# Kernel optimization log

Measured on AMD Instinct MI355X. Metric: run time of the kernel, lower is better.

## Reference

```python
import jax, jax.numpy as jnp
import numpy as np


def _wn(v, g):
    # weight norm over input axis: w[:, j] = g[j] * v[:, j] / ||v[:, j]||
    norm = jnp.sqrt(jnp.sum(v * v, axis=0, keepdims=True))
    return v * (g[None, :] / norm)


def setup_inputs() -> dict:
    key = jax.random.key(0)
    ks = jax.random.split(key, 6)
    M, K1, H, OUT = 65536, 512, 1024, 512
    x = jax.random.normal(ks[0], (M, K1), dtype=jnp.float32)
    v1 = jax.random.normal(ks[1], (K1, H), dtype=jnp.float32) * 0.05
    v2 = jax.random.normal(ks[2], (H, H), dtype=jnp.float32) * 0.05
    v3 = jax.random.normal(ks[3], (H, H), dtype=jnp.float32) * 0.05
    v4 = jax.random.normal(ks[4], (H, H), dtype=jnp.float32) * 0.05
    v5 = jax.random.normal(ks[5], (H, OUT), dtype=jnp.float32) * 0.05
    g1 = jnp.ones((H,), jnp.float32)
    g2 = jnp.ones((H,), jnp.float32)
    g3 = jnp.ones((H,), jnp.float32)
    g4 = jnp.ones((H,), jnp.float32)
    g5 = jnp.ones((OUT,), jnp.float32)
    return {"x": x, "v1": v1, "g1": g1, "v2": v2, "g2": g2,
            "v3": v3, "g3": g3, "v4": v4, "g4": g4, "v5": v5, "g5": g5}


def reference(x, v1, g1, v2, g2, v3, g3, v4, g4, v5, g5):
    w1 = _wn(v1, g1)
    w2 = _wn(v2, g2)
    w3 = _wn(v3, g3)
    w4 = _wn(v4, g4)
    w5 = _wn(v5, g5)
    h1 = jax.nn.softplus(x @ w1)    # [M, H]
    h2 = jax.nn.softplus(h1 @ w2)
    h3 = jax.nn.softplus(h2 @ w3)
    h4 = jax.nn.softplus(h3 @ w4)
    out = h4 @ w5                   # final layer linear
    return out
```

## Files before the change

### kernel.cpp

```cpp
#include <hip/hip_runtime.h>
#include <hip/hip_bf16.h>
#include <cstdint>

typedef unsigned short u16;
typedef __attribute__((ext_vector_type(8))) _Float16 f16x8;
typedef __attribute__((ext_vector_type(4))) float f32x4;
typedef __attribute__((ext_vector_type(8))) unsigned short u16x8;

typedef const __attribute__((address_space(1))) void* gas1p;
typedef __attribute__((address_space(3))) void* las3p;

__device__ __forceinline__ void gld_lds16(const void* g, void* l) {
    __builtin_amdgcn_global_load_lds((gas1p)g, (las3p)l, 16, 0, 0);
}

__device__ __forceinline__ u16 f2h(float f) {
    _Float16 h = (_Float16)f;
    return __builtin_bit_cast(u16, h);
}

__global__ void cvt_x_kernel(const float4* __restrict__ x, u16* __restrict__ xb) {
    size_t i = (size_t)blockIdx.x * blockDim.x + threadIdx.x;
    float4 a = x[2 * i];
    float4 b = x[2 * i + 1];
    u16x8 o;
    o[0] = f2h(a.x); o[1] = f2h(a.y); o[2] = f2h(a.z); o[3] = f2h(a.w);
    o[4] = f2h(b.x); o[5] = f2h(b.y); o[6] = f2h(b.z); o[7] = f2h(b.w);
    *(u16x8*)&xb[i * 8] = o;
}

struct WnDesc {
    const float* v; const float* g; u16* wT; float* partial;
    int K; int N; int blk0;
};
struct WnPack { WnDesc d[5]; int nlayer; };

__global__ void wn_partial_all(WnPack p) {
    int b = blockIdx.x;
    int l = 0;
    while (l + 1 < p.nlayer && b >= p.d[l + 1].blk0) l++;
    const WnDesc& d = p.d[l];
    int lb = b - d.blk0;
    int nbx = d.N >> 6;
    int bx = lb % nbx, seg = lb / nbx;

    int lane = threadIdx.x & 63;
    int tr = threadIdx.x >> 6;
    int n = bx * 64 + lane;
    int kseg = d.K >> 3;
    int kbeg = seg * kseg;
    float s = 0.f;
    for (int k = kbeg + tr; k < kbeg + kseg; k += 4) {
        float x = d.v[(size_t)k * d.N + n];
        s += x * x;
    }
    __shared__ float red[4][64];
    red[tr][lane] = s;
    __syncthreads();
    if (tr == 0)
        d.partial[seg * d.N + n] = red[0][lane] + red[1][lane] + red[2][lane] + red[3][lane];
}

__global__ void wn_write_all(WnPack p) {
    int b = blockIdx.x;
    int l = 0;
    while (l + 1 < p.nlayer && b >= p.d[l + 1].blk0) l++;
    const WnDesc& d = p.d[l];
    int lb = b - d.blk0;
    int nbx = d.N >> 6;
    int bx = lb % nbx, seg = lb / nbx;

    int lane = threadIdx.x & 63;
    int tr = threadIdx.x >> 6;
    int n = bx * 64 + lane;
    float s = 0.f;
#pragma unroll
    for (int i = 0; i < 8; i++) s += d.partial[i * d.N + n];
    float sc = d.g[n] / sqrtf(s);

    int kseg = d.K >> 3;
    int kbeg = seg * kseg;
    for (int k = kbeg + tr; k < kbeg + kseg; k += 4)
        d.wT[(size_t)n * d.K + k] = f2h(d.v[(size_t)k * d.N + n] * sc);
}

template<int N, int K, bool ACT, bool OUTF32>
__global__ __launch_bounds__(512, 2) void gemm_mlp(
    const u16* __restrict__ A, const u16* __restrict__ Bt,
    u16* __restrict__ Ch, float* __restrict__ Cf)
{
    constexpr int M = 65536;
    constexpr int NT = K / 64;
    constexpr int J = NT / 2;
    constexpr int NTN = N / 256;
    constexpr int NWG = (M / 256) * NTN;

    __shared__ u16 sA[2][256 * 64];
    __shared__ u16 sB[2][2 * 128 * 64];

    const int bid = blockIdx.x;
    const int wk = (bid & 7) * (NWG >> 3) + (bid >> 3);
    const int tm = wk / NTN, tn = wk % NTN;
    const long m0 = (long)tm * 256;
    const int n0 = tn * 256;

    const int tid = threadIdx.x;
    const int lane = tid & 63;
    const int wid = tid >> 6;
    const int wm = (wid >> 2) * 128;
    const int wn = (wid & 3) * 64;

    const int r8 = tid >> 3;
    const int gcol = ((tid & 7) ^ (r8 & 7)) * 8;
    const u16* Abase = A + (m0 + r8) * (size_t)K + gcol;
    const u16* Bbase = Bt + (size_t)(n0 + ((r8 >> 5) * 64 + (r8 & 31))) * K + gcol;
    const int dst8 = tid * 8;

    const u16* Aq0 = Abase;
    const u16* Aq1 = Abase + (size_t)64 * K;
    const u16* Aq2 = Abase + (size_t)128 * K;
    const u16* Aq3 = Abase + (size_t)192 * K;
    const u16* B00 = Bbase;
    const u16* B01 = Bbase + (size_t)128 * K;
    const u16* B10 = Bbase + (size_t)32 * K;
    const u16* B11 = Bbase + (size_t)160 * K;

    auto stA = [&](int buf, const u16* base, int t, int q) {
        gld_lds16(base + (size_t)t * 64, &sA[buf][q * 4096 + dst8]);
    };
    auto stB = [&](int buf, const u16* base, int t, int s, int c) {
        gld_lds16(base + (size_t)t * 64, &sB[buf][s * 8192 + c * 4096 + dst8]);
    };
    auto stA0 = [&](int buf, int t) { stA(buf, Aq0, t, 0); stA(buf, Aq2, t, 2); };
    auto stA1 = [&](int buf, int t) { stA(buf, Aq1, t, 1); stA(buf, Aq3, t, 3); };
    auto stB0 = [&](int buf, int t) { stB(buf, B00, t, 0, 0); stB(buf, B01, t, 0, 1); };
    auto stB1 = [&](int buf, int t) { stB(buf, B10, t, 1, 0); stB(buf, B11, t, 1, 1); };

    const int rbase = lane & 15;
    const int co0 = ((lane >> 4) ^ (lane & 7)) * 8;
    const int arow0 = (wm + rbase) * 64 + co0;
    const int brow0 = ((wn >> 6) * 32 + rbase) * 64 + co0;

    f32x4 acc[8][4] = {};
    f16x8 a[4][2], bq[2][2][2];

    auto ldA = [&](int buf, int qm) {
#pragma unroll
        for (int i = 0; i < 4; i++) {
            int base = arow0 + (qm * 64 + i * 16) * 64;
            a[i][0] = *(const f16x8*)&sA[buf][base];
            a[i][1] = *(const f16x8*)&sA[buf][base ^ 32];
        }
    };
    auto ldB = [&](int buf, int qn) {
#pragma unroll
        for (int j2 = 0; j2 < 2; j2++) {
            int base = brow0 + qn * 8192 + j2 * 1024;
            bq[qn][j2][0] = *(const f16x8*)&sB[buf][base];
            bq[qn][j2][1] = *(const f16x8*)&sB[buf][base ^ 32];
        }
    };
    auto mmaq = [&](int qm, int qn) {
        __builtin_amdgcn_s_setprio(1);
#pragma unroll
        for (int kk = 0; kk < 2; kk++)
#pragma unroll
            for (int i = 0; i < 4; i++)
#pragma unroll
                for (int j2 = 0; j2 < 2; j2++)
                    acc[qm * 4 + i][qn * 2 + j2] = __builtin_amdgcn_mfma_f32_16x16x32_f16(
                        a[i][kk], bq[qn][j2][kk], acc[qm * 4 + i][qn * 2 + j2], 0, 0, 0);
        __builtin_amdgcn_s_setprio(0);
    };
    auto bar = [&]() {
        asm volatile("" ::: "memory");
        __builtin_amdgcn_s_barrier();
        asm volatile("" ::: "memory");
    };

    stA0(0, 0); stB0(0, 0); stB1(0, 0); stA1(0, 0);
    stA0(1, 1); stB0(1, 1); stB1(1, 1); stA1(1, 1);
    asm volatile("s_waitcnt vmcnt(8)" ::: "memory");
    bar();

    for (int j = 0; j < J; j++) {
        const int ta = 2 * j, tb = ta + 1;
        const bool tail = (j > 0);
        const bool full = (j + 1 < J);

        if (tail) stB1(1, tb);
        ldA(0, 0); ldB(0, 0);
        bar();
        mmaq(0, 0);
        if (tail) stA1(1, tb);
        ldB(0, 1);
        bar();
        mmaq(0, 1);
        if (full) stA0(0, ta + 2);
        ldA(0, 1);
        bar();
        mmaq(1, 0);
        if (full) {
            stB0(0, ta + 2);
            asm volatile("s_waitcnt vmcnt(4)" ::: "memory");
        } else {
            asm volatile("s_waitcnt vmcnt(0)" ::: "memory");
        }
        bar();
        mmaq(1, 1);

        if (full) stB1(0, ta + 2);
        ldA(1, 0); ldB(1, 0);
        bar();
        mmaq(0, 0);
        if (full) stA1(0, ta + 2);
        ldB(1, 1);
        bar();
        mmaq(0, 1);
        if (full) stA0(1, tb + 2);
        ldA(1, 1);
        bar();
        mmaq(1, 0);
        if (full) {
            stB0(1, tb + 2);
            asm volatile("s_waitcnt vmcnt(4)" ::: "memory");
            bar();
        }
        mmaq(1, 1);
    }

    const long crow0 = m0 + wm + ((lane >> 4) << 2);
    const int ccol0 = n0 + wn + (lane & 15);
#pragma unroll
    for (int fi = 0; fi < 8; fi++) {
#pragma unroll
        for (int r = 0; r < 4; r++) {
            const size_t rowoff = (size_t)(crow0 + fi * 16 + r) * N;
#pragma unroll
            for (int fj = 0; fj < 4; fj++) {
                float v = acc[fi][fj][r];
                if (ACT) v = fmaxf(v, 0.f) + __logf(1.f + __expf(-fabsf(v)));
                if (OUTF32) Cf[rowoff + ccol0 + fj * 16] = v;
                else        Ch[rowoff + ccol0 + fj * 16] = f2h(v);
            }
        }
    }
}

extern "C" void kernel_launch(void* const* d_in, const int* in_sizes, int n_in,
                              void* d_out, int out_size, void* d_ws, size_t ws_size,
                              hipStream_t stream) {
    const float* x  = (const float*)d_in[0];
    const float* v1 = (const float*)d_in[1];
    const float* g1 = (const float*)d_in[2];
    const float* v2 = (const float*)d_in[3];
    const float* g2 = (const float*)d_in[4];
    const float* v3 = (const float*)d_in[5];
    const float* g3 = (const float*)d_in[6];
    const float* v4 = (const float*)d_in[7];
    const float* g4 = (const float*)d_in[8];
    const float* v5 = (const float*)d_in[9];
    const float* g5 = (const float*)d_in[10];
    float* out = (float*)d_out;

    const int M = 65536;
    char* ws = (char*)d_ws;
    u16* bufA = (u16*)(ws);
    u16* bufB = (u16*)(ws + 0x8000000ULL);
    u16* w1T  = (u16*)(ws + 0x10000000ULL);
    u16* w2T  = w1T + 1024 * 512;
    u16* w3T  = w2T + 1024 * 1024;
    u16* w4T  = w3T + 1024 * 1024;
    u16* w5T  = w4T + 1024 * 1024;
    float* part = (float*)(ws + 0x10800000ULL);

    cvt_x_kernel<<<(M * 512) / (256 * 8), 256, 0, stream>>>((const float4*)x, bufB);

    WnPack pk;
    int cum = 0;
    auto mk = [&](int i, const float* v, const float* g, u16* wT, int K, int N) {
        pk.d[i] = WnDesc{v, g, wT, part + i * 8 * 1024, K, N, cum};
        cum += (N / 64) * 8;
    };
    mk(0, v1, g1, w1T, 512, 1024);
    mk(1, v2, g2, w2T, 1024, 1024);
    mk(2, v3, g3, w3T, 1024, 1024);
    mk(3, v4, g4, w4T, 1024, 1024);
    mk(4, v5, g5, w5T, 1024, 512);
    pk.nlayer = 5;

    wn_partial_all<<<cum, 256, 0, stream>>>(pk);
    wn_write_all<<<cum, 256, 0, stream>>>(pk);

    gemm_mlp<1024, 512,  true,  false><<<1024, 512, 0, stream>>>(bufB, w1T, bufA, nullptr);
    gemm_mlp<1024, 1024, true,  false><<<1024, 512, 0, stream>>>(bufA, w2T, bufB, nullptr);
    gemm_mlp<1024, 1024, true,  false><<<1024, 512, 0, stream>>>(bufB, w3T, bufA, nullptr);
    gemm_mlp<1024, 1024, true,  false><<<1024, 512, 0, stream>>>(bufA, w4T, bufB, nullptr);
    gemm_mlp<512,  1024, false, true ><<<512,  512, 0, stream>>>(bufB, w5T, nullptr, out);

    (void)in_sizes; (void)n_in; (void)out_size; (void)ws_size;
}
```

Before: 721.0 us.

## Restructure GEMM main loop pipeline with peeled last iteration and extra barriers

Rewrites the double-buffered GEMM K-loop schedule. The final iteration is peeled out so the tail/full conditionals disappear, and the global-to-LDS stores are reordered relative to the LDS reads. Explicit lgkmcnt waits and barriers now bracket each MFMA quarter. The goal is a cleaner overlap of global loads, LDS reads and MFMA work, but doubling the barrier count can add synchronisation stalls.

After: 721.3 us. About the same (+0.0%).

```diff
diff --git a/kernel.cpp b/kernel.cpp
--- a/kernel.cpp
+++ b/kernel.cpp
@@ -179,53 +179,88 @@
     };
 
     stA0(0, 0); stB0(0, 0); stB1(0, 0); stA1(0, 0);
-    stA0(1, 1); stB0(1, 1); stB1(1, 1); stA1(1, 1);
-    asm volatile("s_waitcnt vmcnt(8)" ::: "memory");
+    stA0(1, 1); stB0(1, 1); stB1(1, 1);
+    asm volatile("s_waitcnt vmcnt(6)" ::: "memory");
     bar();
 
-    for (int j = 0; j < J; j++) {
+    for (int j = 0; j < J - 1; j++) {
         const int ta = 2 * j, tb = ta + 1;
-        const bool tail = (j > 0);
-        const bool full = (j + 1 < J);
-
-        if (tail) stB1(1, tb);
         ldA(0, 0); ldB(0, 0);
+        stA1(1, tb);
+        asm volatile("s_waitcnt lgkmcnt(8)" ::: "memory");
         bar();
         mmaq(0, 0);
-        if (tail) stA1(1, tb);
+        bar();
         ldB(0, 1);
+        stA0(0, ta + 2);
         bar();
         mmaq(0, 1);
-        if (full) stA0(0, ta + 2);
+        bar();
         ldA(0, 1);
+        stB0(0, ta + 2);
         bar();
         mmaq(1, 0);
-        if (full) {
-            stB0(0, ta + 2);
-            asm volatile("s_waitcnt vmcnt(4)" ::: "memory");
-        } else {
-            asm volatile("s_waitcnt vmcnt(0)" ::: "memory");
-        }
+        bar();
+        stB1(0, ta + 2);
+        asm volatile("s_waitcnt vmcnt(6)" ::: "memory");
         bar();
         mmaq(1, 1);
-
-        if (full) stB1(0, ta + 2);
+        bar();
         ldA(1, 0); ldB(1, 0);
+        stA1(0, ta + 2);
+        asm volatile("s_waitcnt lgkmcnt(8)" ::: "memory");
         bar();
         mmaq(0, 0);
-        if (full) stA1(0, ta + 2);
+        bar();
         ldB(1, 1);
+        stA0(1, tb + 2);
         bar();
         mmaq(0, 1);
-        if (full) stA0(1, tb + 2);
+        bar();
         ldA(1, 1);
+        stB0(1, tb + 2);
         bar();
         mmaq(1, 0);
-        if (full) {
-            stB0(1, tb + 2);
-            asm volatile("s_waitcnt vmcnt(4)" ::: "memory");
-            bar();
-        }
+        bar();
+        stB1(1, tb + 2);
+        asm volatile("s_waitcnt vmcnt(6)" ::: "memory");
+        bar();
+        mmaq(1, 1);
+        bar();
+    }
+
+    {
+        const int tb = NT - 1;
+        ldA(0, 0); ldB(0, 0);
+        stA1(1, tb);
+        asm volatile("s_waitcnt lgkmcnt(8)" ::: "memory");
+        bar();
+        mmaq(0, 0);
+        bar();
+        ldB(0, 1);
+        bar();
+        mmaq(0, 1);
+        bar();
+        ldA(0, 1);
+        bar();
+        mmaq(1, 0);
+        bar();
+        asm volatile("s_waitcnt vmcnt(0)" ::: "memory");
+        bar();
+        mmaq(1, 1);
+        bar();
+        ldA(1, 0); ldB(1, 0);
+        bar();
+        mmaq(0, 0);
+        bar();
+        ldB(1, 1);
+        bar();
+        mmaq(0, 1);
+        bar();
+        ldA(1, 1);
+        bar();
+        mmaq(1, 0);
+        bar();
         mmaq(1, 1);
     }
 
```
